# Kernel tuning notes

Measured on AMD Instinct MI355X. Metric: run time of the kernel, lower is better.

## Reference

```python
import jax, jax.numpy as jnp
import numpy as np

HEADS = 8
DIM_HEAD = 80
BATCH_SIZE = 2  # cfg batch (module init kwarg)


def setup_inputs() -> dict:
    key = jax.random.key(0)
    ks = jax.random.split(key, 6)
    F, S, D = 16, 1024, 640  # frames*batch, latent HW, query_dim
    hidden_states = jax.random.normal(ks[0], (F, S, D), jnp.float32)
    Wq = jax.random.normal(ks[1], (D, D), jnp.float32) * 0.02
    Wk = jax.random.normal(ks[2], (D, D), jnp.float32) * 0.02
    Wv = jax.random.normal(ks[3], (D, D), jnp.float32) * 0.02
    Wo = jax.random.normal(ks[4], (D, D), jnp.float32) * 0.02
    bo = jax.random.normal(ks[5], (D,), jnp.float32) * 0.02
    return {"hidden_states": hidden_states, "Wq": Wq, "Wk": Wk, "Wv": Wv, "Wo": Wo, "bo": bo}


def reference(hidden_states, Wq, Wk, Wv, Wo, bo):
    F, S, D = hidden_states.shape
    h, d = HEADS, DIM_HEAD
    scale = d ** -0.5

    q = hidden_states @ Wq  # [F, S, D]
    k = hidden_states @ Wk
    v = hidden_states @ Wv

    # cross-frame trick: replace every frame's K/V with the FIRST frame of its batch group
    vl = 1 if F < BATCH_SIZE else F // BATCH_SIZE  # video_length
    g = F // vl  # batch groups
    k = jnp.broadcast_to(k.reshape(g, vl, S, D)[:, :1], (g, vl, S, D)).reshape(F, S, D)
    v = jnp.broadcast_to(v.reshape(g, vl, S, D)[:, :1], (g, vl, S, D)).reshape(F, S, D)

    def to_heads(t):  # [F, S, h*d] -> [F*h, S, d]
        return t.reshape(F, S, h, d).transpose(0, 2, 1, 3).reshape(F * h, S, d)

    qh, kh, vh = to_heads(q), to_heads(k), to_heads(v)

    scores = jnp.einsum('bid,bjd->bij', qh, kh) * scale  # [F*h, S, S]
    probs = jax.nn.softmax(scores, axis=-1)
    out = jnp.einsum('bij,bjd->bid', probs, vh)  # [F*h, S, d]

    out = out.reshape(F, h, S, d).transpose(0, 2, 1, 3).reshape(F, S, h * d)
    return out @ Wo + bo
```

## Files before the change

kernel.cpp:

```cpp
#include <hip/hip_runtime.h>
#include <hip/hip_bf16.h>

typedef unsigned short u16;
typedef unsigned int u32;
typedef __attribute__((ext_vector_type(8))) short bf16x8;
typedef __attribute__((ext_vector_type(4))) float f32x4;

#define D640 640

__device__ __forceinline__ float b2f(u16 u) {
  union { u32 i; float f; } x; x.i = ((u32)u) << 16; return x.f;
}
__device__ __forceinline__ u16 f2b(float f) {
  union { __hip_bfloat16 h; u16 u; } c; c.h = __float2bfloat16(f); return c.u;
}
__device__ __forceinline__ u32 pack2(float a, float b) {
  union { __hip_bfloat162 h; u32 u; } c;
  c.h.x = __float2bfloat16(a); c.h.y = __float2bfloat16(b); return c.u;
}
__device__ __forceinline__ bf16x8 pack8(f32x4 lo, f32x4 hi) {
  bf16x8 r;
  r[0] = (short)f2b(lo[0]); r[1] = (short)f2b(lo[1]);
  r[2] = (short)f2b(lo[2]); r[3] = (short)f2b(lo[3]);
  r[4] = (short)f2b(hi[0]); r[5] = (short)f2b(hi[1]);
  r[6] = (short)f2b(hi[2]); r[7] = (short)f2b(hi[3]);
  return r;
}

__global__ void detect_dtype(const u16* __restrict__ hs, u32* __restrict__ flag) {
  __shared__ u32 cnt;
  if (threadIdx.x == 0) cnt = 0;
  __syncthreads();
  int plaus = 0;
#pragma unroll
  for (int i = 0; i < 16; ++i) {
    u16 u = hs[(threadIdx.x * 16 + i) * 2];
    u32 e = (u >> 7) & 0xFF;
    if ((e >= 0x70 && e <= 0x8F) || (u & 0x7FFF) == 0) plaus++;
  }
  atomicAdd(&cnt, (u32)plaus);
  __syncthreads();
  if (threadIdx.x == 0) *flag = (cnt < 2048) ? 1u : 0u;
}

__global__ __launch_bounds__(256) void transpose_w(
    const void* __restrict__ w0, const void* __restrict__ w1,
    const void* __restrict__ w2, const void* __restrict__ w3,
    u16* __restrict__ out, const u32* __restrict__ flag)
{
  __shared__ u16 t[32][33];
  const bool isF32 = (*flag != 0);
  const void* src = blockIdx.z == 0 ? w0 : blockIdx.z == 1 ? w1 : blockIdx.z == 2 ? w2 : w3;
  u16* dst = out + (size_t)blockIdx.z * 409600;
  int tx = threadIdx.x, ty = threadIdx.y;
  int x = blockIdx.x * 32 + tx;
  int y = blockIdx.y * 32 + ty;
  if (isF32) {
    const float* s = (const float*)src;
#pragma unroll
    for (int j = 0; j < 32; j += 8) t[ty + j][tx] = f2b(s[(y + j) * D640 + x]);
  } else {
    const u16* s = (const u16*)src;
#pragma unroll
    for (int j = 0; j < 32; j += 8) t[ty + j][tx] = s[(y + j) * D640 + x];
  }
  __syncthreads();
  int x2 = blockIdx.y * 32 + tx;
  int y2 = blockIdx.x * 32 + ty;
#pragma unroll
  for (int j = 0; j < 32; j += 8) dst[(y2 + j) * D640 + x2] = t[tx][ty + j];
}

__device__ __forceinline__ void gemm_body(
    const void* __restrict__ Av, const u16* __restrict__ BT, void* __restrict__ Cv,
    float scale, const void* __restrict__ bias, bool isF32,
    int aRow0, int aF32mode, int cMode, int bx, int by)
{
  __shared__ __align__(16) u16 Asub[128 * 32];
  __shared__ __align__(16) u16 Bsub[128 * 32];
  const bool aF32 = aF32mode && isF32;
  const bool cF32 = (cMode == 1) && isF32;
  const int tid = threadIdx.x;
  const int lane = tid & 63, w = tid >> 6;
  const int wr = w >> 1, wc = w & 1;
  const int l15 = lane & 15, g = lane >> 4;
  const int rowBase = bx * 128;
  const int colBase = by * 128;

  const int r0 = tid >> 2, r1 = r0 + 64, gc = tid & 3;
  const int ls0 = r0 * 4 + (gc ^ ((r0 >> 1) & 3));
  const int ls1 = r1 * 4 + (gc ^ ((r1 >> 1) & 3));
  const size_t aIdx0 = (size_t)(aRow0 + rowBase + r0) * D640 + gc * 8;
  const size_t aIdx1 = (size_t)(aRow0 + rowBase + r1) * D640 + gc * 8;
  const u16* Bg0 = BT + (colBase + r0) * D640 + gc * 8;
  const u16* Bg1 = BT + (colBase + r1) * D640 + gc * 8;

  int aoff[4], boff[4];
#pragma unroll
  for (int f = 0; f < 4; ++f) {
    int R = wr * 64 + f * 16 + l15;
    aoff[f] = (R * 4 + (g ^ ((R >> 1) & 3))) * 8;
    int Cc = wc * 64 + f * 16 + l15;
    boff[f] = (Cc * 4 + (g ^ ((Cc >> 1) & 3))) * 8;
  }

  f32x4 acc[4][4];
#pragma unroll
  for (int i = 0; i < 4; ++i)
#pragma unroll
    for (int j = 0; j < 4; ++j) acc[i][j] = (f32x4){0.f, 0.f, 0.f, 0.f};

  bf16x8 ra0, ra1, rb0, rb1;
  if (aF32) {
    const float* Af = (const float*)Av;
    ra0 = pack8(*(const f32x4*)(Af + aIdx0), *(const f32x4*)(Af + aIdx0 + 4));
    ra1 = pack8(*(const f32x4*)(Af + aIdx1), *(const f32x4*)(Af + aIdx1 + 4));
  } else {
    const u16* Ab = (const u16*)Av;
    ra0 = *(const bf16x8*)(Ab + aIdx0);
    ra1 = *(const bf16x8*)(Ab + aIdx1);
  }
  rb0 = *(const bf16x8*)Bg0;
  rb1 = *(const bf16x8*)Bg1;

  for (int kt = 0; kt < 20; ++kt) {
    __syncthreads();
    *(bf16x8*)&Asub[ls0 * 8] = ra0;
    *(bf16x8*)&Asub[ls1 * 8] = ra1;
    *(bf16x8*)&Bsub[ls0 * 8] = rb0;
    *(bf16x8*)&Bsub[ls1 * 8] = rb1;
    __syncthreads();
    if (kt < 19) {
      const int k1 = (kt + 1) * 32;
      if (aF32) {
        const float* Af = (const float*)Av;
        ra0 = pack8(*(const f32x4*)(Af + aIdx0 + k1), *(const f32x4*)(Af + aIdx0 + k1 + 4));
        ra1 = pack8(*(const f32x4*)(Af + aIdx1 + k1), *(const f32x4*)(Af + aIdx1 + k1 + 4));
      } else {
        const u16* Ab = (const u16*)Av;
        ra0 = *(const bf16x8*)(Ab + aIdx0 + k1);
        ra1 = *(const bf16x8*)(Ab + aIdx1 + k1);
      }
      rb0 = *(const bf16x8*)(Bg0 + k1);
      rb1 = *(const bf16x8*)(Bg1 + k1);
    }
    bf16x8 a[4], b[4];
#pragma unroll
    for (int f = 0; f < 4; ++f) a[f] = *(const bf16x8*)&Asub[aoff[f]];
#pragma unroll
    for (int f = 0; f < 4; ++f) b[f] = *(const bf16x8*)&Bsub[boff[f]];
    __builtin_amdgcn_s_setprio(1);
#pragma unroll
    for (int i = 0; i < 4; ++i)
#pragma unroll
      for (int j = 0; j < 4; ++j)
        acc[i][j] = __builtin_amdgcn_mfma_f32_16x16x32_bf16(a[i], b[j], acc[i][j], 0, 0, 0);
    __builtin_amdgcn_s_setprio(0);
  }

#pragma unroll
  for (int j = 0; j < 4; ++j) {
    int col = colBase + wc * 64 + j * 16 + l15;
    float bb = 0.f;
    if (bias) bb = cF32 ? ((const float*)bias)[col] : b2f(((const u16*)bias)[col]);
#pragma unroll
    for (int i = 0; i < 4; ++i) {
      int row = rowBase + wr * 64 + i * 16 + g * 4;
#pragma unroll
      for (int r = 0; r < 4; ++r) {
        float v = acc[i][j][r] * scale + bb;
        if (cMode == 2)       ((u16*)Cv)[(size_t)col * 1024 + (row + r)] = f2b(v);
        else if (cF32)        ((float*)Cv)[(size_t)(row + r) * D640 + col] = v;
        else                  ((u16*)Cv)[(size_t)(row + r) * D640 + col] = f2b(v);
      }
    }
  }
}

__global__ __launch_bounds__(256) void gemm_bt(
    const void* __restrict__ Av, const u16* __restrict__ BT, void* __restrict__ Cv,
    float scale, const void* __restrict__ bias, const u32* __restrict__ flag,
    int aRow0, int aF32mode, int cMode)
{
  gemm_body(Av, BT, Cv, scale, bias, (*flag != 0), aRow0, aF32mode, cMode,
            blockIdx.x, blockIdx.y);
}

__global__ __launch_bounds__(256) void gemm_kv(
    const void* __restrict__ hs, const u16* __restrict__ WTk, const u16* __restrict__ WTv,
    u16* __restrict__ Kb, u16* __restrict__ Vb, const u32* __restrict__ flag)
{
  const int z = blockIdx.z;
  const bool isK = (z < 2);
  const int grp = z & 1;
  const u16* bt = isK ? WTk : WTv;
  void* cv = isK ? (void*)(Kb + (size_t)grp * 1024 * 640)
                 : (void*)(Vb + (size_t)grp * 655360);
  gemm_body(hs, bt, cv, 1.f, nullptr, (*flag != 0), grp * 8192, 1, isK ? 0 : 2,
            blockIdx.x, blockIdx.y);
}

__global__ __launch_bounds__(256, 3) void attn_kernel(
    const u16* __restrict__ Q, const u16* __restrict__ K2,
    const u16* __restrict__ VT, u16* __restrict__ AO)
{
  __shared__ __align__(16) u16 Klds[64 * 104];
  __shared__ __align__(16) u16 Vlds[80 * 72];
  __shared__ __align__(16) u16 Plds[4][32 * 72];

  const int tid = threadIdx.x, lane = tid & 63, w = tid >> 6;
  const int l15 = lane & 15, g = lane >> 4;
  const int qc = blockIdx.x, bh = blockIdx.y;
  const int f = bh >> 3, h = bh & 7;
  const int grp = f >> 3;
  u16* Pw = &Plds[w][0];

  const u16* Qp = Q + (size_t)(f * 1024 + qc * 128 + w * 32) * D640 + h * 80;
  const u16* Kp = K2 + (size_t)(grp * 1024) * D640 + h * 80;
  const u16* Vp = VT + (size_t)(grp * 8 + h) * 80 * 1024;

  if (tid < 128) {
    const bf16x8 z8 = {0, 0, 0, 0, 0, 0, 0, 0};
    *(bf16x8*)&Klds[(tid >> 1) * 104 + 80 + (tid & 1) * 8] = z8;
  }

  bf16x8 qreg[2][3];
#pragma unroll
  for (int qb = 0; qb < 2; ++qb)
#pragma unroll
    for (int dc = 0; dc < 3; ++dc) {
      int dd = dc * 32 + g * 8;
      if (dd < 80) qreg[qb][dc] = *(const bf16x8*)(Qp + (l15 + 16 * qb) * D640 + dd);
      else         qreg[qb][dc] = (bf16x8){0, 0, 0, 0, 0, 0, 0, 0};
    }

  f32x4 acc[2][5];
#pragma unroll
  for (int qb = 0; qb < 2; ++qb)
#pragma unroll
    for (int db = 0; db < 5; ++db) acc[qb][db] = (f32x4){0.f, 0.f, 0.f, 0.f};
  float mreg[2] = {-1e30f, -1e30f};
  float lrow[2] = {0.f, 0.f};

  const u16* gsrc[5];
  u16* ldst[5];
  int step[5];
#pragma unroll
  for (int i = 0; i < 5; ++i) {
    int c = tid + i * 256;
    if (c < 640) {
      int row = c / 10, cc = c - row * 10;
      gsrc[i] = Kp + row * D640 + cc * 8;
      ldst[i] = &Klds[row * 104 + cc * 8];
      step[i] = 64 * D640;
    } else {
      int c2 = c - 640, d = c2 >> 3, cc = c2 & 7;
      gsrc[i] = Vp + d * 1024 + cc * 8;
      ldst[i] = &Vlds[d * 72 + cc * 8];
      step[i] = 64;
    }
  }

  bf16x8 pre[5];
#pragma unroll
  for (int i = 0; i < 5; ++i) pre[i] = *(const bf16x8*)gsrc[i];

  for (int it = 0; it < 16; ++it) {
    __syncthreads();
#pragma unroll
    for (int i = 0; i < 5; ++i) *(bf16x8*)ldst[i] = pre[i];
    __syncthreads();
    if (it < 15) {
#pragma unroll
      for (int i = 0; i < 5; ++i) pre[i] = *(const bf16x8*)(gsrc[i] + (it + 1) * step[i]);
    }

    f32x4 st[4][2];
#pragma unroll
    for (int kb = 0; kb < 4; ++kb)
#pragma unroll
      for (int qb = 0; qb < 2; ++qb) st[kb][qb] = (f32x4){0.f, 0.f, 0.f, 0.f};
    __builtin_amdgcn_s_setprio(1);
#pragma unroll
    for (int dc = 0; dc < 3; ++dc)
#pragma unroll
      for (int kb = 0; kb < 4; ++kb) {
        bf16x8 ka = *(const bf16x8*)&Klds[(kb * 16 + l15) * 104 + dc * 32 + g * 8];
        st[kb][0] = __builtin_amdgcn_mfma_f32_16x16x32_bf16(ka, qreg[0][dc], st[kb][0], 0, 0, 0);
        st[kb][1] = __builtin_amdgcn_mfma_f32_16x16x32_bf16(ka, qreg[1][dc], st[kb][1], 0, 0, 0);
      }
    __builtin_amdgcn_s_setprio(0);

    float mt[2];
#pragma unroll
    for (int qb = 0; qb < 2; ++qb) {
      float m01 = fmaxf(fmaxf(st[0][qb][0], st[0][qb][1]), fmaxf(st[0][qb][2], st[0][qb][3]));
      float m23 = fmaxf(fmaxf(st[1][qb][0], st[1][qb][1]), fmaxf(st[1][qb][2], st[1][qb][3]));
      float m45 = fmaxf(fmaxf(st[2][qb][0], st[2][qb][1]), fmaxf(st[2][qb][2], st[2][qb][3]));
      float m67 = fmaxf(fmaxf(st[3][qb][0], st[3][qb][1]), fmaxf(st[3][qb][2], st[3][qb][3]));
      float m = fmaxf(fmaxf(m01, m23), fmaxf(m45, m67));
      m = fmaxf(m, __shfl_xor(m, 16, 64));
      m = fmaxf(m, __shfl_xor(m, 32, 64));
      mt[qb] = m;
    }

    if (__any((mt[0] > mreg[0] + 8.f) || (mt[1] > mreg[1] + 8.f))) {
#pragma unroll
      for (int qb = 0; qb < 2; ++qb) {
        float mn = fmaxf(mreg[qb], mt[qb]);
        float scl = exp2f(mreg[qb] - mn);
        mreg[qb] = mn;
        lrow[qb] *= scl;
        float s_[4];
#pragma unroll
        for (int r = 0; r < 4; ++r)
          s_[r] = __shfl(scl, (lane & 48) | (g * 4 + r), 64);
#pragma unroll
        for (int db = 0; db < 5; ++db)
#pragma unroll
          for (int r = 0; r < 4; ++r) acc[qb][db][r] *= s_[r];
      }
    }

#pragma unroll
    for (int qb = 0; qb < 2; ++qb) {
      float sum = 0.f;
#pragma unroll
      for (int kb = 0; kb < 4; ++kb) {
        float p0 = exp2f(st[kb][qb][0] - mreg[qb]);
        float p1 = exp2f(st[kb][qb][1] - mreg[qb]);
        float p2 = exp2f(st[kb][qb][2] - mreg[qb]);
        float p3 = exp2f(st[kb][qb][3] - mreg[qb]);
        sum += (p0 + p1) + (p2 + p3);
        uint2 pk;
        pk.x = pack2(p0, p1);
        pk.y = pack2(p2, p3);
        *(uint2*)&Pw[(l15 + 16 * qb) * 72 + kb * 16 + g * 4] = pk;
      }
      sum += __shfl_xor(sum, 16, 64);
      sum += __shfl_xor(sum, 32, 64);
      lrow[qb] += sum;
    }

    __builtin_amdgcn_s_setprio(1);
#pragma unroll
    for (int kc = 0; kc < 2; ++kc) {
      bf16x8 pa0 = *(const bf16x8*)&Pw[(l15) * 72 + kc * 32 + g * 8];
      bf16x8 pa1 = *(const bf16x8*)&Pw[(l15 + 16) * 72 + kc * 32 + g * 8];
#pragma unroll
      for (int db = 0; db < 5; ++db) {
        bf16x8 bv = *(const bf16x8*)&Vlds[(db * 16 + l15) * 72 + kc * 32 + g * 8];
        acc[0][db] = __builtin_amdgcn_mfma_f32_16x16x32_bf16(pa0, bv, acc[0][db], 0, 0, 0);
        acc[1][db] = __builtin_amdgcn_mfma_f32_16x16x32_bf16(pa1, bv, acc[1][db], 0, 0, 0);
      }
    }
    __builtin_amdgcn_s_setprio(0);
  }

  u16* Op = AO + (size_t)(f * 1024 + qc * 128 + w * 32) * D640 + h * 80;
#pragma unroll
  for (int qb = 0; qb < 2; ++qb) {
    float i_[4];
#pragma unroll
    for (int r = 0; r < 4; ++r)
      i_[r] = 1.f / __shfl(lrow[qb], (lane & 48) | (g * 4 + r), 64);
#pragma unroll
    for (int db = 0; db < 5; ++db)
#pragma unroll
      for (int r = 0; r < 4; ++r)
        Op[(qb * 16 + g * 4 + r) * D640 + db * 16 + l15] = f2b(acc[qb][db][r] * i_[r]);
  }
}

extern "C" void kernel_launch(void* const* d_in, const int* in_sizes, int n_in,
                              void* d_out, int out_size, void* d_ws, size_t ws_size,
                              hipStream_t stream) {
  (void)in_sizes; (void)n_in; (void)out_size; (void)ws_size;
  const void* hs = d_in[0];
  const void* wq = d_in[1];
  const void* wk = d_in[2];
  const void* wv = d_in[3];
  const void* wo = d_in[4];
  const void* bo = d_in[5];
  u16* ws = (u16*)d_ws;

  u16* WT  = ws;
  u16* Qb  = ws + 1638400;
  u16* Kb  = Qb + 10485760;
  u16* Vb  = Kb + 1310720;
  u16* AOb = Vb + 1310720;
  u32* flag = (u32*)(AOb + 10485760);

  const float QSCALE = 0.11180339887498949f * 1.44269504088896340f;

  detect_dtype<<<1, 256, 0, stream>>>((const u16*)hs, flag);

  transpose_w<<<dim3(20, 20, 4), dim3(32, 8), 0, stream>>>(wq, wk, wv, wo, WT, flag);

  gemm_bt<<<dim3(128, 5), 256, 0, stream>>>(hs, WT, Qb, QSCALE, nullptr, flag, 0, 1, 0);
  gemm_kv<<<dim3(8, 5, 4), 256, 0, stream>>>(hs, WT + 409600, WT + 819200, Kb, Vb, flag);

  attn_kernel<<<dim3(8, 128), 256, 0, stream>>>(Qb, Kb, Vb, AOb);

  gemm_bt<<<dim3(128, 5), 256, 0, stream>>>(AOb, WT + 1228800, d_out, 1.f, bo, flag, 0, 0, 1);
}
```

Baseline: 172.6 us.

## Pre-convert hidden states to bf16, use direct global-to-LDS loads, keep P in registers

Adds a separate pass that converts hidden_states to bf16 once, so the GEMMs read bf16 only. The GEMM tile loads switch from register staging to global_load_lds DMA with a matching swizzle. The software prefetch of the next k-tile is dropped, so loads are now exposed before each compute step. In attention, the P tile is packed straight into MFMA operand registers instead of going through LDS, with V stored in a permuted row order so the layouts match. Row-max and row-sum cross-lane reductions are deferred to the rescale branch and the epilogue.

```diff
diff --git a/kernel.cpp b/kernel.cpp
--- a/kernel.cpp
+++ b/kernel.cpp
@@ -26,6 +26,10 @@
   r[6] = (short)f2b(hi[2]); r[7] = (short)f2b(hi[3]);
   return r;
 }
+__device__ __forceinline__ void gld_lds16(const u16* g, u16* l) {
+  __builtin_amdgcn_global_load_lds((const __attribute__((address_space(1))) u32*)g,
+                                   (__attribute__((address_space(3))) u32*)l, 16, 0, 0);
+}
 
 __global__ void detect_dtype(const u16* __restrict__ hs, u32* __restrict__ flag) {
   __shared__ u32 cnt;
@@ -41,6 +45,18 @@
   atomicAdd(&cnt, (u32)plaus);
   __syncthreads();
   if (threadIdx.x == 0) *flag = (cnt < 2048) ? 1u : 0u;
+}
+
+__global__ __launch_bounds__(256) void conv_hs(
+    const void* __restrict__ hs, u16* __restrict__ out, const u32* __restrict__ flag)
+{
+  const size_t i = ((size_t)blockIdx.x * 256 + threadIdx.x) * 8;
+  if (*flag) {
+    const float* s = (const float*)hs;
+    *(bf16x8*)(out + i) = pack8(*(const f32x4*)(s + i), *(const f32x4*)(s + i + 4));
+  } else {
+    *(bf16x8*)(out + i) = *(const bf16x8*)((const u16*)hs + i);
+  }
 }
 
 __global__ __launch_bounds__(256) void transpose_w(
@@ -71,14 +87,13 @@
   for (int j = 0; j < 32; j += 8) dst[(y2 + j) * D640 + x2] = t[tx][ty + j];
 }
 
-__device__ __forceinline__ void gemm_body(
-    const void* __restrict__ Av, const u16* __restrict__ BT, void* __restrict__ Cv,
+__device__ __forceinline__ void gemm3_body(
+    const u16* __restrict__ A, const u16* __restrict__ BT, void* __restrict__ Cv,
     float scale, const void* __restrict__ bias, bool isF32,
-    int aRow0, int aF32mode, int cMode, int bx, int by)
+    int aRow0, int cMode, int bx, int by)
 {
   __shared__ __align__(16) u16 Asub[128 * 32];
   __shared__ __align__(16) u16 Bsub[128 * 32];
-  const bool aF32 = aF32mode && isF32;
   const bool cF32 = (cMode == 1) && isF32;
   const int tid = threadIdx.x;
   const int lane = tid & 63, w = tid >> 6;
@@ -87,13 +102,15 @@
   const int rowBase = bx * 128;
   const int colBase = by * 128;
 
-  const int r0 = tid >> 2, r1 = r0 + 64, gc = tid & 3;
-  const int ls0 = r0 * 4 + (gc ^ ((r0 >> 1) & 3));
-  const int ls1 = r1 * 4 + (gc ^ ((r1 >> 1) & 3));
-  const size_t aIdx0 = (size_t)(aRow0 + rowBase + r0) * D640 + gc * 8;
-  const size_t aIdx1 = (size_t)(aRow0 + rowBase + r1) * D640 + gc * 8;
-  const u16* Bg0 = BT + (colBase + r0) * D640 + gc * 8;
-  const u16* Bg1 = BT + (colBase + r1) * D640 + gc * 8;
+  const int c0 = w * 128 + lane, c1 = c0 + 64;
+  const u16* Ag0 = A + (size_t)(aRow0 + rowBase + (c0 >> 2)) * D640 + ((c0 & 3) ^ ((c0 >> 3) & 3)) * 8;
+  const u16* Ag1 = A + (size_t)(aRow0 + rowBase + (c1 >> 2)) * D640 + ((c1 & 3) ^ ((c1 >> 3) & 3)) * 8;
+  const u16* Bg0 = BT + (size_t)(colBase + (c0 >> 2)) * D640 + ((c0 & 3) ^ ((c0 >> 3) & 3)) * 8;
+  const u16* Bg1 = BT + (size_t)(colBase + (c1 >> 2)) * D640 + ((c1 & 3) ^ ((c1 >> 3) & 3)) * 8;
+  u16* lA0 = &Asub[w * 1024];
+  u16* lA1 = &Asub[w * 1024 + 512];
+  u16* lB0 = &Bsub[w * 1024];
+  u16* lB1 = &Bsub[w * 1024 + 512];
 
   int aoff[4], boff[4];
 #pragma unroll
@@ -110,40 +127,13 @@
 #pragma unroll
     for (int j = 0; j < 4; ++j) acc[i][j] = (f32x4){0.f, 0.f, 0.f, 0.f};
 
-  bf16x8 ra0, ra1, rb0, rb1;
-  if (aF32) {
-    const float* Af = (const float*)Av;
-    ra0 = pack8(*(const f32x4*)(Af + aIdx0), *(const f32x4*)(Af + aIdx0 + 4));
-    ra1 = pack8(*(const f32x4*)(Af + aIdx1), *(const f32x4*)(Af + aIdx1 + 4));
-  } else {
-    const u16* Ab = (const u16*)Av;
-    ra0 = *(const bf16x8*)(Ab + aIdx0);
-    ra1 = *(const bf16x8*)(Ab + aIdx1);
-  }
-  rb0 = *(const bf16x8*)Bg0;
-  rb1 = *(const bf16x8*)Bg1;
-
   for (int kt = 0; kt < 20; ++kt) {
     __syncthreads();
-    *(bf16x8*)&Asub[ls0 * 8] = ra0;
-    *(bf16x8*)&Asub[ls1 * 8] = ra1;
-    *(bf16x8*)&Bsub[ls0 * 8] = rb0;
-    *(bf16x8*)&Bsub[ls1 * 8] = rb1;
+    gld_lds16(Ag0 + kt * 32, lA0);
+    gld_lds16(Ag1 + kt * 32, lA1);
+    gld_lds16(Bg0 + kt * 32, lB0);
+    gld_lds16(Bg1 + kt * 32, lB1);
     __syncthreads();
-    if (kt < 19) {
-      const int k1 = (kt + 1) * 32;
-      if (aF32) {
-        const float* Af = (const float*)Av;
-        ra0 = pack8(*(const f32x4*)(Af + aIdx0 + k1), *(const f32x4*)(Af + aIdx0 + k1 + 4));
-        ra1 = pack8(*(const f32x4*)(Af + aIdx1 + k1), *(const f32x4*)(Af + aIdx1 + k1 + 4));
-      } else {
-        const u16* Ab = (const u16*)Av;
-        ra0 = *(const bf16x8*)(Ab + aIdx0 + k1);
-        ra1 = *(const bf16x8*)(Ab + aIdx1 + k1);
-      }
-      rb0 = *(const bf16x8*)(Bg0 + k1);
-      rb1 = *(const bf16x8*)(Bg1 + k1);
-    }
     bf16x8 a[4], b[4];
 #pragma unroll
     for (int f = 0; f < 4; ++f) a[f] = *(const bf16x8*)&Asub[aoff[f]];
@@ -169,26 +159,32 @@
 #pragma unroll
       for (int r = 0; r < 4; ++r) {
         float v = acc[i][j][r] * scale + bb;
-        if (cMode == 2)       ((u16*)Cv)[(size_t)col * 1024 + (row + r)] = f2b(v);
-        else if (cF32)        ((float*)Cv)[(size_t)(row + r) * D640 + col] = v;
-        else                  ((u16*)Cv)[(size_t)(row + r) * D640 + col] = f2b(v);
-      }
-    }
-  }
-}
-
-__global__ __launch_bounds__(256) void gemm_bt(
-    const void* __restrict__ Av, const u16* __restrict__ BT, void* __restrict__ Cv,
+        if (cMode == 2) {
+          int rw = row + r;
+          int rl = rw & 63;
+          int slot = (rl & 32) | ((rl & 12) << 1) | (((rl >> 4) & 1) << 2) | (rl & 3);
+          ((u16*)Cv)[(size_t)col * 1024 + (rw & ~63) + slot] = f2b(v);
+        } else if (cF32) {
+          ((float*)Cv)[(size_t)(row + r) * D640 + col] = v;
+        } else {
+          ((u16*)Cv)[(size_t)(row + r) * D640 + col] = f2b(v);
+        }
+      }
+    }
+  }
+}
+
+__global__ __launch_bounds__(256) void gemm3(
+    const u16* __restrict__ A, const u16* __restrict__ BT, void* __restrict__ Cv,
     float scale, const void* __restrict__ bias, const u32* __restrict__ flag,
-    int aRow0, int aF32mode, int cMode)
-{
-  gemm_body(Av, BT, Cv, scale, bias, (*flag != 0), aRow0, aF32mode, cMode,
-            blockIdx.x, blockIdx.y);
+    int aRow0, int cMode)
+{
+  gemm3_body(A, BT, Cv, scale, bias, (*flag != 0), aRow0, cMode, blockIdx.x, blockIdx.y);
 }
 
 __global__ __launch_bounds__(256) void gemm_kv(
-    const void* __restrict__ hs, const u16* __restrict__ WTk, const u16* __restrict__ WTv,
-    u16* __restrict__ Kb, u16* __restrict__ Vb, const u32* __restrict__ flag)
+    const u16* __restrict__ hsb, const u16* __restrict__ WTk, const u16* __restrict__ WTv,
+    u16* __restrict__ Kb, u16* __restrict__ Vb)
 {
   const int z = blockIdx.z;
   const bool isK = (z < 2);
@@ -196,8 +192,8 @@
   const u16* bt = isK ? WTk : WTv;
   void* cv = isK ? (void*)(Kb + (size_t)grp * 1024 * 640)
                  : (void*)(Vb + (size_t)grp * 655360);
-  gemm_body(hs, bt, cv, 1.f, nullptr, (*flag != 0), grp * 8192, 1, isK ? 0 : 2,
-            blockIdx.x, blockIdx.y);
+  gemm3_body(hsb, bt, cv, 1.f, nullptr, false, grp * 8192, isK ? 0 : 2,
+             blockIdx.x, blockIdx.y);
 }
 
 __global__ __launch_bounds__(256, 3) void attn_kernel(
@@ -206,14 +202,12 @@
 {
   __shared__ __align__(16) u16 Klds[64 * 104];
   __shared__ __align__(16) u16 Vlds[80 * 72];
-  __shared__ __align__(16) u16 Plds[4][32 * 72];
 
   const int tid = threadIdx.x, lane = tid & 63, w = tid >> 6;
   const int l15 = lane & 15, g = lane >> 4;
   const int qc = blockIdx.x, bh = blockIdx.y;
   const int f = bh >> 3, h = bh & 7;
   const int grp = f >> 3;
-  u16* Pw = &Plds[w][0];
 
   const u16* Qp = Q + (size_t)(f * 1024 + qc * 128 + w * 32) * D640 + h * 80;
   const u16* Kp = K2 + (size_t)(grp * 1024) * D640 + h * 80;
@@ -239,7 +233,7 @@
   for (int qb = 0; qb < 2; ++qb)
 #pragma unroll
     for (int db = 0; db < 5; ++db) acc[qb][db] = (f32x4){0.f, 0.f, 0.f, 0.f};
-  float mreg[2] = {-1e30f, -1e30f};
+  float mreg[2] = {0.f, 0.f};
   float lrow[2] = {0.f, 0.f};
 
   const u16* gsrc[5];
@@ -298,16 +292,16 @@
       float m23 = fmaxf(fmaxf(st[1][qb][0], st[1][qb][1]), fmaxf(st[1][qb][2], st[1][qb][3]));
       float m45 = fmaxf(fmaxf(st[2][qb][0], st[2][qb][1]), fmaxf(st[2][qb][2], st[2][qb][3]));
       float m67 = fmaxf(fmaxf(st[3][qb][0], st[3][qb][1]), fmaxf(st[3][qb][2], st[3][qb][3]));
-      float m = fmaxf(fmaxf(m01, m23), fmaxf(m45, m67));
-      m = fmaxf(m, __shfl_xor(m, 16, 64));
-      m = fmaxf(m, __shfl_xor(m, 32, 64));
-      mt[qb] = m;
+      mt[qb] = fmaxf(fmaxf(m01, m23), fmaxf(m45, m67));
     }
 
     if (__any((mt[0] > mreg[0] + 8.f) || (mt[1] > mreg[1] + 8.f))) {
 #pragma unroll
       for (int qb = 0; qb < 2; ++qb) {
-        float mn = fmaxf(mreg[qb], mt[qb]);
+        float m = mt[qb];
+        m = fmaxf(m, __shfl_xor(m, 16, 64));
+        m = fmaxf(m, __shfl_xor(m, 32, 64));
+        float mn = fmaxf(mreg[qb], m);
         float scl = exp2f(mreg[qb] - mn);
         mreg[qb] = mn;
         lrow[qb] *= scl;
@@ -322,9 +316,11 @@
       }
     }
 
+    bf16x8 pa[2][2];
 #pragma unroll
     for (int qb = 0; qb < 2; ++qb) {
       float sum = 0.f;
+      u32 wlo[4], whi[4];
 #pragma unroll
       for (int kb = 0; kb < 4; ++kb) {
         float p0 = exp2f(st[kb][qb][0] - mreg[qb]);
@@ -332,26 +328,29 @@
         float p2 = exp2f(st[kb][qb][2] - mreg[qb]);
         float p3 = exp2f(st[kb][qb][3] - mreg[qb]);
         sum += (p0 + p1) + (p2 + p3);
-        uint2 pk;
-        pk.x = pack2(p0, p1);
-        pk.y = pack2(p2, p3);
-        *(uint2*)&Pw[(l15 + 16 * qb) * 72 + kb * 16 + g * 4] = pk;
-      }
-      sum += __shfl_xor(sum, 16, 64);
-      sum += __shfl_xor(sum, 32, 64);
+        wlo[kb] = pack2(p0, p1);
+        whi[kb] = pack2(p2, p3);
+      }
       lrow[qb] += sum;
+#pragma unroll
+      for (int kc = 0; kc < 2; ++kc) {
+        union { u32 u[4]; bf16x8 v; } cvt;
+        cvt.u[0] = wlo[2 * kc];
+        cvt.u[1] = whi[2 * kc];
+        cvt.u[2] = wlo[2 * kc + 1];
+        cvt.u[3] = whi[2 * kc + 1];
+        pa[qb][kc] = cvt.v;
+      }
     }
 
     __builtin_amdgcn_s_setprio(1);
 #pragma unroll
     for (int kc = 0; kc < 2; ++kc) {
-      bf16x8 pa0 = *(const bf16x8*)&Pw[(l15) * 72 + kc * 32 + g * 8];
-      bf16x8 pa1 = *(const bf16x8*)&Pw[(l15 + 16) * 72 + kc * 32 + g * 8];
 #pragma unroll
       for (int db = 0; db < 5; ++db) {
         bf16x8 bv = *(const bf16x8*)&Vlds[(db * 16 + l15) * 72 + kc * 32 + g * 8];
-        acc[0][db] = __builtin_amdgcn_mfma_f32_16x16x32_bf16(pa0, bv, acc[0][db], 0, 0, 0);
-        acc[1][db] = __builtin_amdgcn_mfma_f32_16x16x32_bf16(pa1, bv, acc[1][db], 0, 0, 0);
+        acc[0][db] = __builtin_amdgcn_mfma_f32_16x16x32_bf16(pa[0][kc], bv, acc[0][db], 0, 0, 0);
+        acc[1][db] = __builtin_amdgcn_mfma_f32_16x16x32_bf16(pa[1][kc], bv, acc[1][db], 0, 0, 0);
       }
     }
     __builtin_amdgcn_s_setprio(0);
@@ -360,10 +359,13 @@
   u16* Op = AO + (size_t)(f * 1024 + qc * 128 + w * 32) * D640 + h * 80;
 #pragma unroll
   for (int qb = 0; qb < 2; ++qb) {
+    float lr = lrow[qb];
+    lr += __shfl_xor(lr, 16, 64);
+    lr += __shfl_xor(lr, 32, 64);
     float i_[4];
 #pragma unroll
     for (int r = 0; r < 4; ++r)
-      i_[r] = 1.f / __shfl(lrow[qb], (lane & 48) | (g * 4 + r), 64);
+      i_[r] = 1.f / __shfl(lr, (lane & 48) | (g * 4 + r), 64);
 #pragma unroll
     for (int db = 0; db < 5; ++db)
 #pragma unroll
@@ -388,19 +390,20 @@
   u16* Qb  = ws + 1638400;
   u16* Kb  = Qb + 10485760;
   u16* Vb  = Kb + 1310720;
-  u16* AOb = Vb + 1310720;
-  u32* flag = (u32*)(AOb + 10485760);
+  u16* hsb = Vb + 1310720;
+  u16* AOb = hsb;
+  u32* flag = (u32*)(hsb + 10485760);
 
   const float QSCALE = 0.11180339887498949f * 1.44269504088896340f;
 
   detect_dtype<<<1, 256, 0, stream>>>((const u16*)hs, flag);
-
+  conv_hs<<<5120, 256, 0, stream>>>(hs, hsb, flag);
   transpose_w<<<dim3(20, 20, 4), dim3(32, 8), 0, stream>>>(wq, wk, wv, wo, WT, flag);
 
-  gemm_bt<<<dim3(128, 5), 256, 0, stream>>>(hs, WT, Qb, QSCALE, nullptr, flag, 0, 1, 0);
-  gemm_kv<<<dim3(8, 5, 4), 256, 0, stream>>>(hs, WT + 409600, WT + 819200, Kb, Vb, flag);
+  gemm3<<<dim3(128, 5), 256, 0, stream>>>(hsb, WT, Qb, QSCALE, nullptr, flag, 0, 0);
+  gemm_kv<<<dim3(8, 5, 4), 256, 0, stream>>>(hsb, WT + 409600, WT + 819200, Kb, Vb);
 
   attn_kernel<<<dim3(8, 128), 256, 0, stream>>>(Qb, Kb, Vb, AOb);
 
-  gemm_bt<<<dim3(128, 5), 256, 0, stream>>>(AOb, WT + 1228800, d_out, 1.f, bo, flag, 0, 0, 1);
-}
+  gemm3<<<dim3(128, 5), 256, 0, stream>>>(AOb, WT + 1228800, d_out, 1.f, bo, flag, 0, 1);
+}
```

Result: faster. 165.7 us (-4.0%).
